# Optimization experiments

Measured on AMD Instinct MI355X. Metric: run time of the kernel, lower is better.

## Reference

```python
import jax, jax.numpy as jnp
import numpy as np


def setup_inputs() -> dict:
    key = jax.random.key(0)
    k1, k2, k3 = jax.random.split(key, 3)
    N, E, C, OUT = 100000, 1000000, 64, 64
    x = jax.random.normal(k1, (N, C), dtype=jnp.float32)
    edge_index = jax.random.randint(k2, (2, E), 0, N, dtype=jnp.int32)
    W = jax.random.normal(k3, (2 * C, OUT), dtype=jnp.float32) * (1.0 / np.sqrt(2 * C))
    b = jnp.zeros((OUT,), dtype=jnp.float32)
    return {"x": x, "edge_index": edge_index, "W": W, "b": b}


def reference(x, edge_index, W, b):
    # MRConv: x_j = scatter_max(x[src] - x[dst], dst); out = relu(cat([x, x_j]) @ W + b)
    N = x.shape[0]
    src, dst = edge_index[0], edge_index[1]
    diff = x[src] - x[dst]                                  # [E, C] gather + diff
    x_j = jax.ops.segment_max(diff, dst, num_segments=N)    # [N, C] scatter-max
    # nodes with no incoming edges get -inf from segment_max; tg fills them with 0
    x_j = jnp.where(jnp.isfinite(x_j), x_j, 0.0)
    h = jnp.concatenate([x, x_j], axis=1)                   # [N, 2C]
    return jax.nn.relu(h @ W + b)                           # [N, OUT]
```

## Files before the change

kernel.cpp:

```cpp
#include <hip/hip_runtime.h>
#include <math.h>

#define SENT 0x007FFFFFu
#define NEGINF_BITS 0xFF800000u
#define NA 256
#define SB_SHIFT 5
#define SB_MASK ((1u << SB_SHIFT) - 1u)
#define NB 32
#define PITCH 68
#define MAXSB 4096
#define CGRID 1024

typedef __attribute__((ext_vector_type(8))) short bf16x8;
typedef __attribute__((ext_vector_type(4))) float f32x4;

__device__ __forceinline__ unsigned int fmap(float f) {
    unsigned int u = __float_as_uint(f);
    return (u & 0x80000000u) ? ~u : (u | 0x80000000u);
}
__device__ __forceinline__ unsigned int fmap_bits(unsigned int u) {
    return (u & 0x80000000u) ? ~u : (u | 0x80000000u);
}
__device__ __forceinline__ float funmap(unsigned int u) {
    unsigned int bits = (u & 0x80000000u) ? (u ^ 0x80000000u) : ~u;
    return __uint_as_float(bits);
}
__device__ __forceinline__ unsigned short tobf(float f) {
    unsigned int u = __float_as_uint(f);
    u += 0x7FFFu + ((u >> 16) & 1u);
    return (unsigned short)(u >> 16);
}
__device__ __forceinline__ float frombf(unsigned short s) {
    return __uint_as_float((unsigned int)s << 16);
}

__global__ void __launch_bounds__(256) casthist_kernel(const float* __restrict__ x,
                                                       unsigned short* __restrict__ xb,
                                                       long long n,
                                                       const int* __restrict__ ei,
                                                       unsigned* __restrict__ counts2,
                                                       int E, int nsb, int chunk, int cgrid) {
    __shared__ unsigned h[MAXSB];
    if ((int)blockIdx.x < cgrid) {
        long long i = ((long long)blockIdx.x * 256 + threadIdx.x) * 8;
        long long stride = (long long)cgrid * 256 * 8;
        for (; i < n; i += stride) {
            float4 a = *(const float4*)(x + i);
            float4 c = *(const float4*)(x + i + 4);
            uint4 o;
            o.x = (unsigned)tobf(a.x) | ((unsigned)tobf(a.y) << 16);
            o.y = (unsigned)tobf(a.z) | ((unsigned)tobf(a.w) << 16);
            o.z = (unsigned)tobf(c.x) | ((unsigned)tobf(c.y) << 16);
            o.w = (unsigned)tobf(c.z) | ((unsigned)tobf(c.w) << 16);
            *(uint4*)(xb + i) = o;
        }
    } else {
        int hb = (int)blockIdx.x - cgrid;
        for (int t = threadIdx.x; t < nsb; t += 256) h[t] = 0u;
        __syncthreads();
        int beg = hb * chunk;
        int end = min(beg + chunk, E);
        for (int i = beg + threadIdx.x; i < end; i += 256)
            atomicAdd(&h[((unsigned)ei[E + i]) >> SB_SHIFT], 1u);
        __syncthreads();
        for (int t = threadIdx.x; t < nsb; t += 256)
            counts2[(size_t)t * NA + hb] = h[t];
    }
}

__global__ void __launch_bounds__(256) histA_kernel(const int* __restrict__ ei,
                                                    unsigned* __restrict__ counts2,
                                                    int E, int nsb, int chunk) {
    __shared__ unsigned h[MAXSB];
    for (int t = threadIdx.x; t < nsb; t += 256) h[t] = 0u;
    __syncthreads();
    int beg = blockIdx.x * chunk;
    int end = min(beg + chunk, E);
    for (int i = beg + threadIdx.x; i < end; i += 256)
        atomicAdd(&h[((unsigned)ei[E + i]) >> SB_SHIFT], 1u);
    __syncthreads();
    for (int t = threadIdx.x; t < nsb; t += 256)
        counts2[(size_t)t * NA + blockIdx.x] = h[t];
}

__global__ void __launch_bounds__(512) rowscan_kernel(unsigned* __restrict__ counts2,
                                                      unsigned* __restrict__ sbtot, int nsb) {
    int lane = threadIdx.x & 63;
    int sb = blockIdx.x * 8 + (threadIdx.x >> 6);
    if (sb >= nsb) return;
    unsigned* row = counts2 + (size_t)sb * NA;
    uint4 v = *(const uint4*)(row + 4 * lane);
    unsigned local = v.x + v.y + v.z + v.w;
    unsigned incl = local;
    #pragma unroll
    for (int d = 1; d < 64; d <<= 1) {
        unsigned t = __shfl_up(incl, d);
        if (lane >= d) incl += t;
    }
    unsigned e0 = incl - local;
    uint4 o;
    o.x = e0;
    o.y = e0 + v.x;
    o.z = o.y + v.y;
    o.w = o.z + v.z;
    *(uint4*)(row + 4 * lane) = o;
    if (lane == 63) sbtot[sb] = incl;
}

__global__ void __launch_bounds__(1024) sbscan_kernel(const unsigned* __restrict__ sbtot,
                                                      unsigned* __restrict__ sbbase, int nsb) {
    __shared__ unsigned s[1024];
    __shared__ unsigned carry_s;
    if (threadIdx.x == 0) carry_s = 0u;
    __syncthreads();
    for (int chunk = 0; chunk < nsb; chunk += 1024) {
        int i = chunk + threadIdx.x;
        unsigned v = (i < nsb) ? sbtot[i] : 0u;
        s[threadIdx.x] = v;
        __syncthreads();
        for (int d = 1; d < 1024; d <<= 1) {
            unsigned t = (threadIdx.x >= d) ? s[threadIdx.x - d] : 0u;
            __syncthreads();
            s[threadIdx.x] += t;
            __syncthreads();
        }
        unsigned carry = carry_s;
        if (i < nsb) sbbase[i] = carry + s[threadIdx.x] - v;
        __syncthreads();
        if (threadIdx.x == 1023) carry_s = carry + s[1023];
        __syncthreads();
    }
    if (threadIdx.x == 0) sbbase[nsb] = carry_s;
}

__global__ void __launch_bounds__(256) placeB_kernel(const int* __restrict__ ei,
                                                     const unsigned* __restrict__ counts2,
                                                     const unsigned* __restrict__ sbbase,
                                                     unsigned* __restrict__ ssrc,
                                                     int E, int nsb, int chunk) {
    __shared__ unsigned fill[MAXSB];
    for (int t = threadIdx.x; t < nsb; t += 256)
        fill[t] = sbbase[t] + counts2[(size_t)t * NA + blockIdx.x];
    __syncthreads();
    int beg = blockIdx.x * chunk;
    int end = min(beg + chunk, E);
    for (int i = beg + threadIdx.x; i < end; i += 256) {
        unsigned src = (unsigned)ei[i];
        unsigned dst = (unsigned)ei[E + i];
        unsigned pos = atomicAdd(&fill[dst >> SB_SHIFT], 1u);
        ssrc[pos] = (src << SB_SHIFT) | (dst & SB_MASK);
    }
}

__global__ void __launch_bounds__(256) reduceBf_kernel(const unsigned short* __restrict__ xb,
                                                       const unsigned* __restrict__ sbbase,
                                                       const unsigned* __restrict__ ssrc,
                                                       unsigned short* __restrict__ xj, int N) {
    __shared__ unsigned M[NB * PITCH];
    int tid = threadIdx.x;
    int lane = tid & 63;
    int wid = tid >> 6;

    for (int i = tid; i < NB * PITCH; i += 256) M[i] = SENT;

    int nodeBase = blockIdx.x * NB;
    int beg = (int)sbbase[blockIdx.x];
    int end = (int)sbbase[blockIdx.x + 1];
    __syncthreads();

    for (int i0 = beg + wid * 64; i0 < end; i0 += 256) {
        int i = i0 + lane;
        unsigned p = (i < end) ? __builtin_nontemporal_load(&ssrc[i]) : 0u;
        int cnt = min(64, end - i0);
        unsigned pfirst = __shfl(p, 0);
        for (int j = 0; j < cnt; j += 16) {
            unsigned pp[16];
            unsigned uu[16];
            #pragma unroll
            for (int k = 0; k < 16; ++k) {
                pp[k] = (j + k < cnt) ? __shfl(p, j + k) : pfirst;
                uu[k] = (unsigned)xb[(size_t)(pp[k] >> SB_SHIFT) * 64 + lane] << 16;
            }
            #pragma unroll
            for (int k = 0; k < 16; ++k)
                atomicMax(&M[(pp[k] & SB_MASK) * PITCH + lane], fmap_bits(uu[k]));
        }
    }
    __syncthreads();

    for (int row = wid; row < NB; row += 4) {
        int n = nodeBase + row;
        if (n < N) {
            unsigned um = M[row * PITCH + lane];
            unsigned short o = 0;
            if (um != SENT) {
                float mx = funmap(um);
                float xv = frombf(xb[(size_t)n * 64 + lane]);
                o = tobf(mx - xv);
            }
            xj[(size_t)n * 64 + lane] = o;
        }
    }
}

__global__ void __launch_bounds__(256) mlpBf_kernel(const unsigned short* __restrict__ xb,
                                                    const unsigned short* __restrict__ xj,
                                                    const float* __restrict__ W,
                                                    const float* __restrict__ b,
                                                    float* __restrict__ out, int N) {
    int lane = threadIdx.x & 63;
    int wid  = threadIdx.x >> 6;
    int r = lane & 15;
    int g = lane >> 4;

    bf16x8 Bf[4][4];
    #pragma unroll
    for (int nt = 0; nt < 4; ++nt)
        #pragma unroll
        for (int kt = 0; kt < 4; ++kt) {
            const float* wp = W + (size_t)(kt * 32 + g * 8) * 64 + nt * 16 + r;
            bf16x8 f;
            #pragma unroll
            for (int j = 0; j < 8; ++j) f[j] = (short)tobf(wp[(size_t)j * 64]);
            Bf[nt][kt] = f;
        }
    float bias[4];
    #pragma unroll
    for (int nt = 0; nt < 4; ++nt) bias[nt] = b[nt * 16 + r];

    int nTiles = (N + 15) >> 4;
    int totalWaves = gridDim.x * 4;
    for (int tile = blockIdx.x * 4 + wid; tile < nTiles; tile += totalWaves) {
        int nodeBase = tile << 4;
        int rowIdx = min(nodeBase + r, N - 1);
        const unsigned short* xp = xb + (size_t)rowIdx * 64;
        const unsigned short* jp = xj + (size_t)rowIdx * 64;

        bf16x8 Af[4];
        #pragma unroll
        for (int kt = 0; kt < 2; ++kt) {
            Af[kt]     = *(const bf16x8*)(xp + kt * 32 + g * 8);
            Af[2 + kt] = *(const bf16x8*)(jp + kt * 32 + g * 8);
        }

        f32x4 acc[4];
        #pragma unroll
        for (int nt = 0; nt < 4; ++nt) {
            f32x4 a = {bias[nt], bias[nt], bias[nt], bias[nt]};
            acc[nt] = a;
        }
        #pragma unroll
        for (int nt = 0; nt < 4; ++nt)
            #pragma unroll
            for (int kt = 0; kt < 4; ++kt)
                acc[nt] = __builtin_amdgcn_mfma_f32_16x16x32_bf16(Af[kt], Bf[nt][kt], acc[nt], 0, 0, 0);

        #pragma unroll
        for (int nt = 0; nt < 4; ++nt)
            #pragma unroll
            for (int reg = 0; reg < 4; ++reg) {
                int nrow = nodeBase + g * 4 + reg;
                if (nrow < N)
                    out[(size_t)nrow * 64 + nt * 16 + r] = fmaxf(acc[nt][reg], 0.0f);
            }
    }
}


__global__ void __launch_bounds__(256) reduceB_kernel(const float* __restrict__ x,
                                                      const unsigned* __restrict__ sbbase,
                                                      const unsigned* __restrict__ ssrc,
                                                      float* __restrict__ xj, int N) {
    __shared__ unsigned M[NB * PITCH];
    int tid = threadIdx.x;
    int lane = tid & 63;
    int wid = tid >> 6;

    for (int i = tid; i < NB * PITCH; i += 256) M[i] = SENT;

    int nodeBase = blockIdx.x * NB;
    int beg = (int)sbbase[blockIdx.x];
    int end = (int)sbbase[blockIdx.x + 1];
    __syncthreads();

    for (int i0 = beg + wid * 64; i0 < end; i0 += 256) {
        int i = i0 + lane;
        unsigned p = (i < end) ? ssrc[i] : 0u;
        int cnt = min(64, end - i0);
        unsigned pfirst = __shfl(p, 0);
        for (int j = 0; j < cnt; j += 16) {
            unsigned pp[16];
            float vv[16];
            #pragma unroll
            for (int k = 0; k < 16; ++k) {
                pp[k] = (j + k < cnt) ? __shfl(p, j + k) : pfirst;
                vv[k] = x[(size_t)(pp[k] >> SB_SHIFT) * 64 + lane];
            }
            #pragma unroll
            for (int k = 0; k < 16; ++k)
                atomicMax(&M[(pp[k] & SB_MASK) * PITCH + lane], fmap(vv[k]));
        }
    }
    __syncthreads();

    for (int row = wid; row < NB; row += 4) {
        int n = nodeBase + row;
        if (n < N) xj[(size_t)n * 64 + lane] = funmap(M[row * PITCH + lane]);
    }
}

template <bool MAPPED>
__global__ void __launch_bounds__(256) mlp_kernel(const float* __restrict__ x,
                                                  const unsigned int* xj,
                                                  const float* __restrict__ W,
                                                  const float* __restrict__ b,
                                                  float* out, int N) {
    int lane = threadIdx.x & 63;
    int wid  = threadIdx.x >> 6;
    int r = lane & 15;
    int g = lane >> 4;

    bf16x8 Bf[4][4];
    #pragma unroll
    for (int nt = 0; nt < 4; ++nt)
        #pragma unroll
        for (int kt = 0; kt < 4; ++kt) {
            const float* wp = W + (size_t)(kt * 32 + g * 8) * 64 + nt * 16 + r;
            bf16x8 f;
            #pragma unroll
            for (int j = 0; j < 8; ++j) f[j] = (short)tobf(wp[(size_t)j * 64]);
            Bf[nt][kt] = f;
        }
    float bias[4];
    #pragma unroll
    for (int nt = 0; nt < 4; ++nt) bias[nt] = b[nt * 16 + r];

    int nTiles = (N + 15) >> 4;
    int totalWaves = gridDim.x * 4;
    for (int tile = blockIdx.x * 4 + wid; tile < nTiles; tile += totalWaves) {
        int nodeBase = tile << 4;
        int rowIdx = min(nodeBase + r, N - 1);
        const float* xp = x + (size_t)rowIdx * 64;
        const unsigned int* jp = xj + (size_t)rowIdx * 64;

        bf16x8 Af[4];
        float xs[2][8];
        #pragma unroll
        for (int kt = 0; kt < 2; ++kt) {
            float4 flo = *(const float4*)(xp + kt * 32 + g * 8);
            float4 fhi = *(const float4*)(xp + kt * 32 + g * 8 + 4);
            xs[kt][0] = flo.x; xs[kt][1] = flo.y; xs[kt][2] = flo.z; xs[kt][3] = flo.w;
            xs[kt][4] = fhi.x; xs[kt][5] = fhi.y; xs[kt][6] = fhi.z; xs[kt][7] = fhi.w;
            bf16x8 f;
            #pragma unroll
            for (int j = 0; j < 8; ++j) f[j] = (short)tobf(xs[kt][j]);
            Af[kt] = f;
        }
        #pragma unroll
        for (int kt = 0; kt < 2; ++kt) {
            uint4 ulo = *(const uint4*)(jp + kt * 32 + g * 8);
            uint4 uhi = *(const uint4*)(jp + kt * 32 + g * 8 + 4);
            unsigned int uu[8] = {ulo.x, ulo.y, ulo.z, ulo.w, uhi.x, uhi.y, uhi.z, uhi.w};
            bf16x8 f;
            #pragma unroll
            for (int j = 0; j < 8; ++j) {
                bool empty;
                float v;
                if (MAPPED) { empty = (uu[j] == SENT); v = funmap(uu[j]); }
                else        { empty = (uu[j] == NEGINF_BITS); v = __uint_as_float(uu[j]); }
                f[j] = (short)tobf(empty ? 0.0f : (v - xs[kt][j]));
            }
            Af[2 + kt] = f;
        }

        f32x4 acc[4];
        #pragma unroll
        for (int nt = 0; nt < 4; ++nt) {
            f32x4 a = {bias[nt], bias[nt], bias[nt], bias[nt]};
            acc[nt] = a;
        }
        #pragma unroll
        for (int nt = 0; nt < 4; ++nt)
            #pragma unroll
            for (int kt = 0; kt < 4; ++kt)
                acc[nt] = __builtin_amdgcn_mfma_f32_16x16x32_bf16(Af[kt], Bf[nt][kt], acc[nt], 0, 0, 0);

        #pragma unroll
        for (int nt = 0; nt < 4; ++nt)
            #pragma unroll
            for (int reg = 0; reg < 4; ++reg) {
                int nrow = nodeBase + g * 4 + reg;
                if (nrow < N)
                    out[(size_t)nrow * 64 + nt * 16 + r] = fmaxf(acc[nt][reg], 0.0f);
            }
    }
}


__global__ void init_kernel(uint4* __restrict__ ws, int n4) {
    int i = blockIdx.x * blockDim.x + threadIdx.x;
    int stride = gridDim.x * blockDim.x;
    uint4 v = make_uint4(SENT, SENT, SENT, SENT);
    for (; i < n4; i += stride) ws[i] = v;
}

__global__ void scatter_kernel(const float* __restrict__ x,
                               const int* __restrict__ ei,
                               unsigned int* __restrict__ ws, int E) {
    long long gid = (long long)blockIdx.x * blockDim.x + threadIdx.x;
    int e = (int)(gid >> 6);
    int lane = (int)(gid & 63);
    if (e >= E) return;
    int src = ei[e];
    int dst = ei[E + e];
    unsigned int m = fmap(x[(size_t)src * 64 + lane]);
    unsigned int* p = ws + (size_t)dst * 64 + lane;
    if (m > *p) atomicMax(p, m);
}

extern "C" void kernel_launch(void* const* d_in, const int* in_sizes, int n_in,
                              void* d_out, int out_size, void* d_ws, size_t ws_size,
                              hipStream_t stream) {
    const float* x  = (const float*)d_in[0];
    const int*   ei = (const int*)d_in[1];
    const float* W  = (const float*)d_in[2];
    const float* b  = (const float*)d_in[3];
    float* out = (float*)d_out;

    int N = in_sizes[0] / 64;
    int E = in_sizes[1] / 2;

    int nsb = (N + NB - 1) >> SB_SHIFT;
    int chunk = (E + NA - 1) / NA;

    size_t counts2_b = (size_t)nsb * NA * 4;
    size_t sbtot_b   = (size_t)((nsb + 63) & ~63) * 4;
    size_t sbbase_b  = (size_t)(nsb + 1 + 63) / 64 * 64 * 4;
    size_t ssrc_b    = (size_t)E * 4;
    size_t xb_b      = (size_t)N * 64 * 2;
    size_t xjb_b     = (size_t)N * 64 * 2;
    size_t xj32_b    = (size_t)N * 64 * 4;
    size_t needB     = counts2_b + sbtot_b + sbbase_b + ssrc_b;
    size_t needA     = needB + xb_b + xjb_b;

    int mgrid = (((N + 15) >> 4) + 3) / 4;

    if (ws_size >= needA && nsb <= MAXSB) {
        char* p = (char*)d_ws;
        unsigned* counts2 = (unsigned*)p; p += counts2_b;
        unsigned* sbtot   = (unsigned*)p; p += sbtot_b;
        unsigned* sbbase  = (unsigned*)p; p += sbbase_b;
        unsigned* ssrc    = (unsigned*)p; p += ssrc_b;
        unsigned short* xb  = (unsigned short*)p; p += xb_b;
        unsigned short* xjb = (unsigned short*)p;

        long long n = (long long)N * 64;
        casthist_kernel<<<CGRID + NA, 256, 0, stream>>>(x, xb, n, ei, counts2, E, nsb, chunk, CGRID);
        rowscan_kernel<<<(nsb + 7) / 8, 512, 0, stream>>>(counts2, sbtot, nsb);
        sbscan_kernel<<<1, 1024, 0, stream>>>(sbtot, sbbase, nsb);
        placeB_kernel<<<NA, 256, 0, stream>>>(ei, counts2, sbbase, ssrc, E, nsb, chunk);
        reduceBf_kernel<<<nsb, 256, 0, stream>>>(xb, sbbase, ssrc, xjb, N);
        mlpBf_kernel<<<mgrid, 256, 0, stream>>>(xb, xjb, W, b, out, N);
    } else if (ws_size >= needB && nsb <= MAXSB) {
        char* p = (char*)d_ws;
        unsigned* counts2 = (unsigned*)p; p += counts2_b;
        unsigned* sbtot   = (unsigned*)p; p += sbtot_b;
        unsigned* sbbase  = (unsigned*)p; p += sbbase_b;
        unsigned* ssrc    = (unsigned*)p; p += ssrc_b;
        float* xjp = (ws_size >= needB + xj32_b) ? (float*)p : (float*)d_out;

        histA_kernel<<<NA, 256, 0, stream>>>(ei, counts2, E, nsb, chunk);
        rowscan_kernel<<<(nsb + 7) / 8, 512, 0, stream>>>(counts2, sbtot, nsb);
        sbscan_kernel<<<1, 1024, 0, stream>>>(sbtot, sbbase, nsb);
        placeB_kernel<<<NA, 256, 0, stream>>>(ei, counts2, sbbase, ssrc, E, nsb, chunk);
        reduceB_kernel<<<nsb, 256, 0, stream>>>(x, sbbase, ssrc, xjp, N);
        mlp_kernel<false><<<mgrid, 256, 0, stream>>>(x, (const unsigned*)xjp, W, b, out, N);
    } else {
        size_t need2 = (size_t)N * 64 * 4;
        unsigned int* scratch = (ws_size >= need2) ? (unsigned int*)d_ws : (unsigned int*)d_out;
        init_kernel<<<2048, 256, 0, stream>>>((uint4*)scratch, N * 16);
        long long sthreads = (long long)E * 64;
        int sblocks = (int)((sthreads + 255) / 256);
        scatter_kernel<<<sblocks, 256, 0, stream>>>(x, ei, scratch, E);
        mlp_kernel<true><<<mgrid, 256, 0, stream>>>(x, scratch, W, b, out, N);
    }
}
```

Measured before the change: 104.1 us.

## Pad superblock edge lists to 16 and load packed edges as uniform vectors

Measured after the change: 103.8 us. Within noise of the previous version (-0.3%).

```diff
diff --git a/kernel.cpp b/kernel.cpp
--- a/kernel.cpp
+++ b/kernel.cpp
@@ -10,6 +10,7 @@
 #define PITCH 68
 #define MAXSB 4096
 #define CGRID 1024
+#define PADROW 32u
 
 typedef __attribute__((ext_vector_type(8))) short bf16x8;
 typedef __attribute__((ext_vector_type(4))) float f32x4;
@@ -115,7 +116,7 @@
     __syncthreads();
     for (int chunk = 0; chunk < nsb; chunk += 1024) {
         int i = chunk + threadIdx.x;
-        unsigned v = (i < nsb) ? sbtot[i] : 0u;
+        unsigned v = (i < nsb) ? ((sbtot[i] + 15u) & ~15u) : 0u;
         s[threadIdx.x] = v;
         __syncthreads();
         for (int d = 1; d < 1024; d <<= 1) {
@@ -148,42 +149,52 @@
         unsigned src = (unsigned)ei[i];
         unsigned dst = (unsigned)ei[E + i];
         unsigned pos = atomicAdd(&fill[dst >> SB_SHIFT], 1u);
-        ssrc[pos] = (src << SB_SHIFT) | (dst & SB_MASK);
-    }
+        ssrc[pos] = (src << 6) | (dst & SB_MASK);
+    }
+}
+
+__global__ void __launch_bounds__(256) pad_kernel(const unsigned* __restrict__ sbbase,
+                                                  const unsigned* __restrict__ sbtot,
+                                                  unsigned* __restrict__ ssrc, int nsb) {
+    int i = blockIdx.x * blockDim.x + threadIdx.x;
+    if (i >= nsb) return;
+    unsigned s = sbbase[i] + sbtot[i];
+    unsigned e = sbbase[i + 1];
+    for (unsigned j = s; j < e; ++j) ssrc[j] = PADROW;
 }
 
 __global__ void __launch_bounds__(256) reduceBf_kernel(const unsigned short* __restrict__ xb,
                                                        const unsigned* __restrict__ sbbase,
                                                        const unsigned* __restrict__ ssrc,
                                                        unsigned short* __restrict__ xj, int N) {
-    __shared__ unsigned M[NB * PITCH];
+    __shared__ unsigned M[(NB + 1) * PITCH];
     int tid = threadIdx.x;
     int lane = tid & 63;
     int wid = tid >> 6;
 
-    for (int i = tid; i < NB * PITCH; i += 256) M[i] = SENT;
+    for (int i = tid; i < (NB + 1) * PITCH; i += 256) M[i] = SENT;
 
     int nodeBase = blockIdx.x * NB;
     int beg = (int)sbbase[blockIdx.x];
     int end = (int)sbbase[blockIdx.x + 1];
     __syncthreads();
 
-    for (int i0 = beg + wid * 64; i0 < end; i0 += 256) {
-        int i = i0 + lane;
-        unsigned p = (i < end) ? __builtin_nontemporal_load(&ssrc[i]) : 0u;
-        int cnt = min(64, end - i0);
-        unsigned pfirst = __shfl(p, 0);
-        for (int j = 0; j < cnt; j += 16) {
-            unsigned pp[16];
-            unsigned uu[16];
-            #pragma unroll
-            for (int k = 0; k < 16; ++k) {
-                pp[k] = (j + k < cnt) ? __shfl(p, j + k) : pfirst;
-                uu[k] = (unsigned)xb[(size_t)(pp[k] >> SB_SHIFT) * 64 + lane] << 16;
-            }
-            #pragma unroll
-            for (int k = 0; k < 16; ++k)
-                atomicMax(&M[(pp[k] & SB_MASK) * PITCH + lane], fmap_bits(uu[k]));
+    for (int i0 = beg + wid * 16; i0 < end; i0 += 64) {
+        int si = __builtin_amdgcn_readfirstlane(i0);
+        uint4 q0 = *(const uint4*)(ssrc + si);
+        uint4 q1 = *(const uint4*)(ssrc + si + 4);
+        uint4 q2 = *(const uint4*)(ssrc + si + 8);
+        uint4 q3 = *(const uint4*)(ssrc + si + 12);
+        unsigned pp[16] = {q0.x, q0.y, q0.z, q0.w, q1.x, q1.y, q1.z, q1.w,
+                           q2.x, q2.y, q2.z, q2.w, q3.x, q3.y, q3.z, q3.w};
+        unsigned short vv[16];
+        #pragma unroll
+        for (int k = 0; k < 16; ++k)
+            vv[k] = xb[(pp[k] & 0xFFFFFFC0u) | (unsigned)lane];
+        #pragma unroll
+        for (int k = 0; k < 16; ++k) {
+            unsigned u32 = ((unsigned)vv[k]) << 16;
+            atomicMax(&M[(pp[k] & 63u) * PITCH + lane], fmap_bits(u32));
         }
     }
     __syncthreads();
@@ -271,35 +282,33 @@
                                                       const unsigned* __restrict__ sbbase,
                                                       const unsigned* __restrict__ ssrc,
                                                       float* __restrict__ xj, int N) {
-    __shared__ unsigned M[NB * PITCH];
+    __shared__ unsigned M[(NB + 1) * PITCH];
     int tid = threadIdx.x;
     int lane = tid & 63;
     int wid = tid >> 6;
 
-    for (int i = tid; i < NB * PITCH; i += 256) M[i] = SENT;
+    for (int i = tid; i < (NB + 1) * PITCH; i += 256) M[i] = SENT;
 
     int nodeBase = blockIdx.x * NB;
     int beg = (int)sbbase[blockIdx.x];
     int end = (int)sbbase[blockIdx.x + 1];
     __syncthreads();
 
-    for (int i0 = beg + wid * 64; i0 < end; i0 += 256) {
-        int i = i0 + lane;
-        unsigned p = (i < end) ? ssrc[i] : 0u;
-        int cnt = min(64, end - i0);
-        unsigned pfirst = __shfl(p, 0);
-        for (int j = 0; j < cnt; j += 16) {
-            unsigned pp[16];
-            float vv[16];
-            #pragma unroll
-            for (int k = 0; k < 16; ++k) {
-                pp[k] = (j + k < cnt) ? __shfl(p, j + k) : pfirst;
-                vv[k] = x[(size_t)(pp[k] >> SB_SHIFT) * 64 + lane];
-            }
-            #pragma unroll
-            for (int k = 0; k < 16; ++k)
-                atomicMax(&M[(pp[k] & SB_MASK) * PITCH + lane], fmap(vv[k]));
-        }
+    for (int i0 = beg + wid * 16; i0 < end; i0 += 64) {
+        int si = __builtin_amdgcn_readfirstlane(i0);
+        uint4 q0 = *(const uint4*)(ssrc + si);
+        uint4 q1 = *(const uint4*)(ssrc + si + 4);
+        uint4 q2 = *(const uint4*)(ssrc + si + 8);
+        uint4 q3 = *(const uint4*)(ssrc + si + 12);
+        unsigned pp[16] = {q0.x, q0.y, q0.z, q0.w, q1.x, q1.y, q1.z, q1.w,
+                           q2.x, q2.y, q2.z, q2.w, q3.x, q3.y, q3.z, q3.w};
+        float vv[16];
+        #pragma unroll
+        for (int k = 0; k < 16; ++k)
+            vv[k] = x[(pp[k] & 0xFFFFFFC0u) | (unsigned)lane];
+        #pragma unroll
+        for (int k = 0; k < 16; ++k)
+            atomicMax(&M[(pp[k] & 63u) * PITCH + lane], fmap(vv[k]));
     }
     __syncthreads();
 
@@ -436,7 +445,7 @@
     size_t counts2_b = (size_t)nsb * NA * 4;
     size_t sbtot_b   = (size_t)((nsb + 63) & ~63) * 4;
     size_t sbbase_b  = (size_t)(nsb + 1 + 63) / 64 * 64 * 4;
-    size_t ssrc_b    = (size_t)E * 4;
+    size_t ssrc_b    = ((size_t)E + 16u * (size_t)nsb) * 4;
     size_t xb_b      = (size_t)N * 64 * 2;
     size_t xjb_b     = (size_t)N * 64 * 2;
     size_t xj32_b    = (size_t)N * 64 * 4;
@@ -459,6 +468,7 @@
         rowscan_kernel<<<(nsb + 7) / 8, 512, 0, stream>>>(counts2, sbtot, nsb);
         sbscan_kernel<<<1, 1024, 0, stream>>>(sbtot, sbbase, nsb);
         placeB_kernel<<<NA, 256, 0, stream>>>(ei, counts2, sbbase, ssrc, E, nsb, chunk);
+        pad_kernel<<<(nsb + 255) / 256, 256, 0, stream>>>(sbbase, sbtot, ssrc, nsb);
         reduceBf_kernel<<<nsb, 256, 0, stream>>>(xb, sbbase, ssrc, xjb, N);
         mlpBf_kernel<<<mgrid, 256, 0, stream>>>(xb, xjb, W, b, out, N);
     } else if (ws_size >= needB && nsb <= MAXSB) {
@@ -473,6 +483,7 @@
         rowscan_kernel<<<(nsb + 7) / 8, 512, 0, stream>>>(counts2, sbtot, nsb);
         sbscan_kernel<<<1, 1024, 0, stream>>>(sbtot, sbbase, nsb);
         placeB_kernel<<<NA, 256, 0, stream>>>(ei, counts2, sbbase, ssrc, E, nsb, chunk);
+        pad_kernel<<<(nsb + 255) / 256, 256, 0, stream>>>(sbbase, sbtot, ssrc, nsb);
         reduceB_kernel<<<nsb, 256, 0, stream>>>(x, sbbase, ssrc, xjp, N);
         mlp_kernel<false><<<mgrid, 256, 0, stream>>>(x, (const unsigned*)xjp, W, b, out, N);
     } else {
```
